# Kernel optimization log

Hardware: AMD Instinct MI355X
Metric: run time of the kernel (lower is better)

Reference implementation:

```python
import jax, jax.numpy as jnp
import numpy as np

EMBED_DIM = 1024
BATCH = 4
SEQ = 2048


def setup_inputs() -> dict:
    key = jax.random.key(0)
    ks = jax.random.split(key, 9)
    E = EMBED_DIM
    s = 1.0 / np.sqrt(E)
    inp = {
        "x": jax.random.normal(ks[0], (BATCH, SEQ, E), dtype=jnp.float32),
        "Wq": jax.random.uniform(ks[1], (E, E), jnp.float32, -s, s),
        "bq": jax.random.uniform(ks[2], (E,), jnp.float32, -s, s),
        "Wk": jax.random.uniform(ks[3], (E, E), jnp.float32, -s, s),
        "bk": jax.random.uniform(ks[4], (E,), jnp.float32, -s, s),
        "Wv": jax.random.uniform(ks[5], (E, E), jnp.float32, -s, s),
        "bv": jax.random.uniform(ks[6], (E,), jnp.float32, -s, s),
        "Wo": jax.random.uniform(ks[7], (E, E), jnp.float32, -s, s),
        "bo": jax.random.uniform(ks[8], (E,), jnp.float32, -s, s),
    }
    return inp


def reference(x, Wq, bq, Wk, bk, Wv, bv, Wo, bo):
    # x: [B, S, E]. Single-head attention over full embed_dim.
    scale = x.shape[-1] ** -0.5
    q = jnp.einsum("bse,ef->bsf", x, Wq.T) + bq
    k = jnp.einsum("bse,ef->bsf", x, Wk.T) + bk
    v = jnp.einsum("bse,ef->bsf", x, Wv.T) + bv
    scores = jnp.einsum("bqe,bke->bqk", q, k) * scale  # [B, S, S]
    attn = jax.nn.softmax(scores, axis=-1)             # dropout p=0 -> identity
    out = jnp.einsum("bqk,bke->bqe", attn, v)
    return jnp.einsum("bse,ef->bsf", out, Wo.T) + bo
```

## Files before the change

### kernel.cpp

```cpp
#include <hip/hip_runtime.h>
#include <hip/hip_bf16.h>


typedef __bf16 bf16_t;
typedef __bf16 bf16x8 __attribute__((ext_vector_type(8)));
typedef __bf16 bf16x4 __attribute__((ext_vector_type(4)));
typedef float  f32x16 __attribute__((ext_vector_type(16)));

__device__ __forceinline__ void async_copy16(const void* g, void* l) {
  __builtin_amdgcn_global_load_lds(
      (const __attribute__((address_space(1))) void*)g,
      (__attribute__((address_space(3))) void*)l, 16, 0, 0);
}

__device__ __forceinline__ void store_out(float* p, float v)  { *p = v; }
__device__ __forceinline__ void store_out(bf16_t* p, float v) { *p = (bf16_t)v; }

#define BM 128
#define BN 128
#define BKT 64

template <typename OutT, int BIAS, int EPI>
__global__ __launch_bounds__(256) void gemm_bt(
    const bf16_t* __restrict__ A, const bf16_t* __restrict__ B,
    OutT* __restrict__ C,
    const float* __restrict__ b0, const float* __restrict__ b1,
    float* __restrict__ rsum, int rsStride,
    int M, int N, int K, int lda, int ldb, int ldc, float scale,
    long long strideA, long long strideB, long long strideC) {
  const int z = blockIdx.z;
  A += (long long)z * strideA;
  B += (long long)z * strideB;
  C += (long long)z * strideC;
  if (EPI >= 1) rsum += (long long)z * rsStride;

  int bx = blockIdx.x, by = blockIdx.y;
  {
    const int GX  = gridDim.x;
    const int id  = by * GX + bx;
    const int per = GX * 8;
    const int grp = id / per;
    const int rem = id - grp * per;
    by = grp * 8 + (rem & 7);
    bx = rem >> 3;
  }

  __shared__ __align__(16) bf16_t As[BM * BKT];
  __shared__ __align__(16) bf16_t Bs[BN * BKT];

  const int t    = threadIdx.x;
  const int lane = t & 63;
  const int w    = t >> 6;
  const int wm   = w & 1;
  const int wn   = w >> 1;
  const int tileM = by * BM;
  const int tileN = bx * BN;

  f32x16 acc[2][2] = {};

  for (int k0 = 0; k0 < K; k0 += BKT) {
#pragma unroll
    for (int i = 0; i < 4; ++i) {
      const int c   = t + 256 * i;
      const int row = c >> 3;
      const int cc  = c & 7;
      const int gcc = cc ^ (row & 7);
      const int ldsbase = ((t & ~63) + 256 * i) * 8;
      async_copy16(A + (long long)(tileM + row) * lda + k0 + gcc * 8, &As[ldsbase]);
      async_copy16(B + (long long)(tileN + row) * ldb + k0 + gcc * 8, &Bs[ldsbase]);
    }
    __syncthreads();

#pragma unroll
    for (int s = 0; s < 4; ++s) {
      const int kc = s + 4 * (lane >> 5);
      bf16x8 af[2], bfr[2];
#pragma unroll
      for (int ti = 0; ti < 2; ++ti) {
        const int row = wm * 64 + ti * 32 + (lane & 31);
        af[ti] = *(const bf16x8*)&As[row * BKT + ((kc ^ (row & 7)) * 8)];
      }
#pragma unroll
      for (int tj = 0; tj < 2; ++tj) {
        const int row = wn * 64 + tj * 32 + (lane & 31);
        bfr[tj] = *(const bf16x8*)&Bs[row * BKT + ((kc ^ (row & 7)) * 8)];
      }
#pragma unroll
      for (int ti = 0; ti < 2; ++ti)
#pragma unroll
        for (int tj = 0; tj < 2; ++tj)
          acc[ti][tj] = __builtin_amdgcn_mfma_f32_32x32x16_bf16(
              af[ti], bfr[tj], acc[ti][tj], 0, 0, 0);
    }
    __syncthreads();
  }

  if (EPI == 0 && BIAS != 3) {
#pragma unroll
    for (int tj = 0; tj < 2; ++tj) {
      const int col = tileN + wn * 64 + tj * 32 + (lane & 31);
      float bv = 0.f;
      if (BIAS == 1) bv = b0[col];
      if (BIAS == 2) bv = (col < 1024 ? b0[col] : b1[col - 1024]);
#pragma unroll
      for (int ti = 0; ti < 2; ++ti) {
        const int rowb = tileM + wm * 64 + ti * 32 + 4 * (lane >> 5);
#pragma unroll
        for (int r = 0; r < 16; ++r) {
          const int row = rowb + (r & 3) + 8 * (r >> 2);
          store_out(&C[(long long)row * ldc + col], acc[ti][tj][r] * scale + bv);
        }
      }
    }
  } else {
    const int col0 = tileN + wn * 64 + (lane & 31);
#pragma unroll
    for (int ti = 0; ti < 2; ++ti) {
      const int rowb = tileM + wm * 64 + ti * 32 + 4 * (lane >> 5);
#pragma unroll
      for (int r = 0; r < 16; ++r) {
        const int row = rowb + (r & 3) + 8 * (r >> 2);
        if (EPI == 1) {
          const float e0 = __expf(acc[ti][0][r] * scale);
          const float e1 = __expf(acc[ti][1][r] * scale);
          store_out(&C[(long long)row * ldc + col0],      e0);
          store_out(&C[(long long)row * ldc + col0 + 32], e1);
          float s = e0 + e1;
          s += __shfl_xor(s, 1);  s += __shfl_xor(s, 2);
          s += __shfl_xor(s, 4);  s += __shfl_xor(s, 8);
          s += __shfl_xor(s, 16);
          if ((lane & 31) == 0) atomicAdd(&rsum[row], s);
        } else if (EPI == 2) {
          const float inv = 1.0f / rsum[row];
          store_out(&C[(long long)row * ldc + col0],      acc[ti][0][r] * inv);
          store_out(&C[(long long)row * ldc + col0 + 32], acc[ti][1][r] * inv);
        } else {
          const float bv = b0[row];
          store_out(&C[(long long)row * ldc + col0],      acc[ti][0][r] * scale + bv);
          store_out(&C[(long long)row * ldc + col0 + 32], acc[ti][1][r] * scale + bv);
        }
      }
    }
  }
}

__global__ __launch_bounds__(256) void cast_all(
    const float4* __restrict__ w0, const float4* __restrict__ w1,
    const float4* __restrict__ w2, const float4* __restrict__ w3,
    const float4* __restrict__ x,
    bf16x4* __restrict__ wdst, bf16x4* __restrict__ xdst,
    float4* __restrict__ rsumv4) {
  const int N4W  = 1 << 18;
  const int BASE = 4 * N4W + (1 << 21);
  const int id = blockIdx.x * 256 + threadIdx.x;
  if (id >= BASE) {
    const int i = id - BASE;
    if (i < 2048) rsumv4[i] = make_float4(0.f, 0.f, 0.f, 0.f);
    return;
  }
  const float4* src;
  bf16x4* dst;
  if (id < 4 * N4W) {
    const int zz = id >> 18;
    src = (zz == 0 ? w0 : zz == 1 ? w1 : zz == 2 ? w2 : w3) + (id & (N4W - 1));
    dst = wdst + id;
  } else {
    const int i = id - 4 * N4W;
    src = x + i;
    dst = xdst + i;
  }
  const float4 v = *src;
  bf16x4 o;
  o[0] = (bf16_t)v.x; o[1] = (bf16_t)v.y; o[2] = (bf16_t)v.z; o[3] = (bf16_t)v.w;
  *dst = o;
}

extern "C" void kernel_launch(void* const* d_in, const int* in_sizes, int n_in,
                              void* d_out, int out_size, void* d_ws, size_t ws_size,
                              hipStream_t stream) {
  const int E = 1024, S = 2048, B = 4;
  const int BS = B * S;

  const float* x  = (const float*)d_in[0];
  const float* Wq = (const float*)d_in[1];
  const float* bq = (const float*)d_in[2];
  const float* Wk = (const float*)d_in[3];
  const float* bk = (const float*)d_in[4];
  const float* Wv = (const float*)d_in[5];
  const float* bv = (const float*)d_in[6];
  const float* Wo = (const float*)d_in[7];
  const float* bo = (const float*)d_in[8];
  float* out = (float*)d_out;

  char* w = (char*)d_ws;
  const size_t MB = 1ull << 20;
  bf16_t* Wqkvb = (bf16_t*)(w + 0 * MB);
  bf16_t* Wvb   = Wqkvb + 2 * E * E;
  bf16_t* Wob   = Wqkvb + 3 * E * E;
  bf16_t* xb    = (bf16_t*)(w + 8 * MB);
  bf16_t* Ob    = (bf16_t*)(w + 8 * MB);
  bf16_t* QKb   = (bf16_t*)(w + 24 * MB);
  bf16_t* VTb   = (bf16_t*)(w + 56 * MB);
  bf16_t* Sb    = (bf16_t*)(w + 72 * MB);
  float*  rsum  = (float*)(w + 104 * MB);

  {
    const int blocks = ((4 << 18) + (1 << 21) + 2048) / 256;
    cast_all<<<blocks, 256, 0, stream>>>(
        (const float4*)Wq, (const float4*)Wk, (const float4*)Wv,
        (const float4*)Wo, (const float4*)x,
        (bf16x4*)Wqkvb, (bf16x4*)xb, (float4*)rsum);
  }

  gemm_bt<bf16_t, 2, 0><<<dim3(2 * E / BN, BS / BM, 1), 256, 0, stream>>>(
      xb, Wqkvb, QKb, bq, bk, nullptr, 0,
      BS, 2 * E, E, E, E, 2 * E, 1.f, 0, 0, 0);

  gemm_bt<bf16_t, 3, 0><<<dim3(BS / BN, E / BM, 1), 256, 0, stream>>>(
      Wvb, xb, VTb, bv, nullptr, nullptr, 0,
      E, BS, E, E, E, BS, 1.f, 0, 0, 0);

  gemm_bt<bf16_t, 0, 1><<<dim3(S / BN, S / BM, B), 256, 0, stream>>>(
      QKb, QKb + E, Sb, nullptr, nullptr, rsum, S,
      S, S, E, 2 * E, 2 * E, S, 0.03125f,
      (long long)S * 2 * E, (long long)S * 2 * E, (long long)S * S);

  gemm_bt<bf16_t, 0, 2><<<dim3(E / BN, S / BM, B), 256, 0, stream>>>(
      Sb, VTb, Ob, nullptr, nullptr, rsum, S,
      S, E, S, S, BS, E, 1.f,
      (long long)S * S, (long long)S, (long long)S * E);

  gemm_bt<float, 1, 0><<<dim3(E / BN, BS / BM, 1), 256, 0, stream>>>(
      Ob, Wob, out, bo, nullptr, nullptr, 0,
      BS, E, E, E, E, E, 1.f, 0, 0, 0);
}
```

Before: 318.5 us.

## Compute softmax row sums via ones-matrix MFMA and defer normalization to output GEMM

The scores epilogue no longer does shuffle reductions and atomicAdd row sums. Instead, the PV kernel gets an extra block column that multiplies the exp-score matrix by an all-ones LDS tile to produce the row sums. Normalization by 1/rowsum moves out of the PV epilogue into the output-projection epilogue, using the identity diag(1/r)·(PV)·Wo. The Q/K and V projections are also merged into one launch, and rsum zeroing is dropped. The trade-offs are extra MFMA work on the ones tile and unnormalized bf16 intermediates.

Result: no change. 321.1 us (+0.8%).

```diff
diff --git a/kernel.cpp b/kernel.cpp
--- a/kernel.cpp
+++ b/kernel.cpp
@@ -20,41 +20,33 @@
 #define BN 128
 #define BKT 64
 
-template <typename OutT, int BIAS, int EPI>
-__global__ __launch_bounds__(256) void gemm_bt(
+__device__ __forceinline__ void supertile(int id, int GX, int& bx, int& by) {
+  const int per = GX * 8;
+  const int grp = id / per;
+  const int rem = id - grp * per;
+  by = grp * 8 + (rem & 7);
+  bx = rem >> 3;
+}
+
+template <typename OutT, int BIAS, int EPI, bool ONES>
+__device__ __forceinline__ void gemm_core(
     const bf16_t* __restrict__ A, const bf16_t* __restrict__ B,
-    OutT* __restrict__ C,
-    const float* __restrict__ b0, const float* __restrict__ b1,
-    float* __restrict__ rsum, int rsStride,
-    int M, int N, int K, int lda, int ldb, int ldc, float scale,
-    long long strideA, long long strideB, long long strideC) {
-  const int z = blockIdx.z;
-  A += (long long)z * strideA;
-  B += (long long)z * strideB;
-  C += (long long)z * strideC;
-  if (EPI >= 1) rsum += (long long)z * rsStride;
-
-  int bx = blockIdx.x, by = blockIdx.y;
-  {
-    const int GX  = gridDim.x;
-    const int id  = by * GX + bx;
-    const int per = GX * 8;
-    const int grp = id / per;
-    const int rem = id - grp * per;
-    by = grp * 8 + (rem & 7);
-    bx = rem >> 3;
-  }
-
-  __shared__ __align__(16) bf16_t As[BM * BKT];
-  __shared__ __align__(16) bf16_t Bs[BN * BKT];
-
+    OutT* __restrict__ C, const float* __restrict__ b0,
+    const float* __restrict__ b1, float* __restrict__ rsum,
+    int K, int lda, int ldb, int ldc, float scale,
+    int tileM, int tileN, bf16_t* As, bf16_t* Bs) {
   const int t    = threadIdx.x;
   const int lane = t & 63;
   const int w    = t >> 6;
   const int wm   = w & 1;
   const int wn   = w >> 1;
-  const int tileM = by * BM;
-  const int tileN = bx * BN;
+
+  if (ONES) {
+    bf16x8 ones8;
+#pragma unroll
+    for (int j = 0; j < 8; ++j) ones8[j] = (bf16_t)1.0f;
+    for (int i = t; i < BN * BKT / 8; i += 256) ((bf16x8*)Bs)[i] = ones8;
+  }
 
   f32x16 acc[2][2] = {};
 
@@ -67,7 +59,8 @@
       const int gcc = cc ^ (row & 7);
       const int ldsbase = ((t & ~63) + 256 * i) * 8;
       async_copy16(A + (long long)(tileM + row) * lda + k0 + gcc * 8, &As[ldsbase]);
-      async_copy16(B + (long long)(tileN + row) * ldb + k0 + gcc * 8, &Bs[ldsbase]);
+      if (!ONES)
+        async_copy16(B + (long long)(tileN + row) * ldb + k0 + gcc * 8, &Bs[ldsbase]);
     }
     __syncthreads();
 
@@ -95,7 +88,56 @@
     __syncthreads();
   }
 
-  if (EPI == 0 && BIAS != 3) {
+  if (EPI == 4) {
+    if (wn == 0 && (lane & 31) == 0) {
+#pragma unroll
+      for (int ti = 0; ti < 2; ++ti) {
+        const int rowb = tileM + wm * 64 + ti * 32 + 4 * (lane >> 5);
+#pragma unroll
+        for (int r = 0; r < 16; ++r)
+          rsum[rowb + (r & 3) + 8 * (r >> 2)] = acc[ti][0][r];
+      }
+    }
+  } else if (EPI == 1) {
+    const int col0 = tileN + wn * 64 + (lane & 31);
+#pragma unroll
+    for (int ti = 0; ti < 2; ++ti) {
+      const int rowb = tileM + wm * 64 + ti * 32 + 4 * (lane >> 5);
+#pragma unroll
+      for (int r = 0; r < 16; ++r) {
+        const int row = rowb + (r & 3) + 8 * (r >> 2);
+        store_out(&C[(long long)row * ldc + col0],      __expf(acc[ti][0][r] * scale));
+        store_out(&C[(long long)row * ldc + col0 + 32], __expf(acc[ti][1][r] * scale));
+      }
+    }
+  } else if (EPI == 3) {
+    const int col0 = tileN + wn * 64 + (lane & 31);
+    const float bv0 = b0[col0], bv1 = b0[col0 + 32];
+#pragma unroll
+    for (int ti = 0; ti < 2; ++ti) {
+      const int rowb = tileM + wm * 64 + ti * 32 + 4 * (lane >> 5);
+#pragma unroll
+      for (int r = 0; r < 16; ++r) {
+        const int row = rowb + (r & 3) + 8 * (r >> 2);
+        const float inv = 1.0f / rsum[row];
+        store_out(&C[(long long)row * ldc + col0],      acc[ti][0][r] * inv + bv0);
+        store_out(&C[(long long)row * ldc + col0 + 32], acc[ti][1][r] * inv + bv1);
+      }
+    }
+  } else if (BIAS == 3) {
+    const int col0 = tileN + wn * 64 + (lane & 31);
+#pragma unroll
+    for (int ti = 0; ti < 2; ++ti) {
+      const int rowb = tileM + wm * 64 + ti * 32 + 4 * (lane >> 5);
+#pragma unroll
+      for (int r = 0; r < 16; ++r) {
+        const int row = rowb + (r & 3) + 8 * (r >> 2);
+        const float bv = b0[row];
+        store_out(&C[(long long)row * ldc + col0],      acc[ti][0][r] * scale + bv);
+        store_out(&C[(long long)row * ldc + col0 + 32], acc[ti][1][r] * scale + bv);
+      }
+    }
+  } else {
 #pragma unroll
     for (int tj = 0; tj < 2; ++tj) {
       const int col = tileN + wn * 64 + tj * 32 + (lane & 31);
@@ -112,52 +154,80 @@
         }
       }
     }
-  } else {
-    const int col0 = tileN + wn * 64 + (lane & 31);
-#pragma unroll
-    for (int ti = 0; ti < 2; ++ti) {
-      const int rowb = tileM + wm * 64 + ti * 32 + 4 * (lane >> 5);
-#pragma unroll
-      for (int r = 0; r < 16; ++r) {
-        const int row = rowb + (r & 3) + 8 * (r >> 2);
-        if (EPI == 1) {
-          const float e0 = __expf(acc[ti][0][r] * scale);
-          const float e1 = __expf(acc[ti][1][r] * scale);
-          store_out(&C[(long long)row * ldc + col0],      e0);
-          store_out(&C[(long long)row * ldc + col0 + 32], e1);
-          float s = e0 + e1;
-          s += __shfl_xor(s, 1);  s += __shfl_xor(s, 2);
-          s += __shfl_xor(s, 4);  s += __shfl_xor(s, 8);
-          s += __shfl_xor(s, 16);
-          if ((lane & 31) == 0) atomicAdd(&rsum[row], s);
-        } else if (EPI == 2) {
-          const float inv = 1.0f / rsum[row];
-          store_out(&C[(long long)row * ldc + col0],      acc[ti][0][r] * inv);
-          store_out(&C[(long long)row * ldc + col0 + 32], acc[ti][1][r] * inv);
-        } else {
-          const float bv = b0[row];
-          store_out(&C[(long long)row * ldc + col0],      acc[ti][0][r] * scale + bv);
-          store_out(&C[(long long)row * ldc + col0 + 32], acc[ti][1][r] * scale + bv);
-        }
-      }
-    }
-  }
+  }
+}
+
+#define LDS_DECL \
+  __shared__ __align__(16) bf16_t As[BM * BKT]; \
+  __shared__ __align__(16) bf16_t Bs[BN * BKT];
+
+__global__ __launch_bounds__(256) void proj_kernel(
+    const bf16_t* __restrict__ xb, const bf16_t* __restrict__ Wqkb,
+    const bf16_t* __restrict__ Wvb, bf16_t* __restrict__ QKb,
+    bf16_t* __restrict__ VTb, const float* __restrict__ bq,
+    const float* __restrict__ bk, const float* __restrict__ bv) {
+  LDS_DECL;
+  const int id = blockIdx.x;
+  if (id < 1024) {
+    int bx, by; supertile(id, 16, bx, by);
+    gemm_core<bf16_t, 2, 0, false>(xb, Wqkb, QKb, bq, bk, nullptr,
+        1024, 1024, 1024, 2048, 1.f, by * 128, bx * 128, As, Bs);
+  } else {
+    int bx, by; supertile(id - 1024, 64, bx, by);
+    gemm_core<bf16_t, 3, 0, false>(Wvb, xb, VTb, bv, nullptr, nullptr,
+        1024, 1024, 1024, 8192, 1.f, by * 128, bx * 128, As, Bs);
+  }
+}
+
+__global__ __launch_bounds__(256) void scores_kernel(
+    const bf16_t* __restrict__ QKb, bf16_t* __restrict__ Sb) {
+  LDS_DECL;
+  const int z = blockIdx.z;
+  const bf16_t* A = QKb + (long long)z * 2048 * 2048;
+  const bf16_t* Bm = A + 1024;
+  bf16_t* C = Sb + (long long)z * 2048 * 2048;
+  int bx, by; supertile(blockIdx.y * 16 + blockIdx.x, 16, bx, by);
+  gemm_core<bf16_t, 0, 1, false>(A, Bm, C, nullptr, nullptr, nullptr,
+      1024, 2048, 2048, 2048, 0.03125f, by * 128, bx * 128, As, Bs);
+}
+
+__global__ __launch_bounds__(256) void pv_kernel(
+    const bf16_t* __restrict__ Sb, const bf16_t* __restrict__ VTb,
+    bf16_t* __restrict__ Ob, float* __restrict__ rsum) {
+  LDS_DECL;
+  const int z = blockIdx.z;
+  const bf16_t* A = Sb + (long long)z * 2048 * 2048;
+  const bf16_t* Bm = VTb + (long long)z * 2048;
+  bf16_t* C = Ob + (long long)z * 2048 * 1024;
+  float* rs = rsum + z * 2048;
+  if (blockIdx.x == 8) {
+    gemm_core<bf16_t, 0, 4, true>(A, nullptr, C, nullptr, nullptr, rs,
+        2048, 2048, 0, 1024, 1.f, blockIdx.y * 128, 0, As, Bs);
+  } else {
+    int bx, by; supertile(blockIdx.y * 8 + blockIdx.x, 8, bx, by);
+    gemm_core<bf16_t, 0, 0, false>(A, Bm, C, nullptr, nullptr, nullptr,
+        2048, 2048, 8192, 1024, 1.f, by * 128, bx * 128, As, Bs);
+  }
+}
+
+__global__ __launch_bounds__(256) void out_kernel(
+    const bf16_t* __restrict__ Ob, const bf16_t* __restrict__ Wob,
+    float* __restrict__ out, const float* __restrict__ bo,
+    const float* __restrict__ rsum) {
+  LDS_DECL;
+  int bx, by; supertile(blockIdx.y * 8 + blockIdx.x, 8, bx, by);
+  gemm_core<float, 1, 3, false>(Ob, Wob, out, bo, nullptr,
+      const_cast<float*>(rsum),
+      1024, 1024, 1024, 1024, 1.f, by * 128, bx * 128, As, Bs);
 }
 
 __global__ __launch_bounds__(256) void cast_all(
     const float4* __restrict__ w0, const float4* __restrict__ w1,
     const float4* __restrict__ w2, const float4* __restrict__ w3,
     const float4* __restrict__ x,
-    bf16x4* __restrict__ wdst, bf16x4* __restrict__ xdst,
-    float4* __restrict__ rsumv4) {
-  const int N4W  = 1 << 18;
-  const int BASE = 4 * N4W + (1 << 21);
+    bf16x4* __restrict__ wdst, bf16x4* __restrict__ xdst) {
+  const int N4W = 1 << 18;
   const int id = blockIdx.x * 256 + threadIdx.x;
-  if (id >= BASE) {
-    const int i = id - BASE;
-    if (i < 2048) rsumv4[i] = make_float4(0.f, 0.f, 0.f, 0.f);
-    return;
-  }
   const float4* src;
   bf16x4* dst;
   if (id < 4 * N4W) {
@@ -194,43 +264,25 @@
 
   char* w = (char*)d_ws;
   const size_t MB = 1ull << 20;
-  bf16_t* Wqkvb = (bf16_t*)(w + 0 * MB);
-  bf16_t* Wvb   = Wqkvb + 2 * E * E;
-  bf16_t* Wob   = Wqkvb + 3 * E * E;
-  bf16_t* xb    = (bf16_t*)(w + 8 * MB);
-  bf16_t* Ob    = (bf16_t*)(w + 8 * MB);
-  bf16_t* QKb   = (bf16_t*)(w + 24 * MB);
-  bf16_t* VTb   = (bf16_t*)(w + 56 * MB);
-  bf16_t* Sb    = (bf16_t*)(w + 72 * MB);
-  float*  rsum  = (float*)(w + 104 * MB);
-
-  {
-    const int blocks = ((4 << 18) + (1 << 21) + 2048) / 256;
-    cast_all<<<blocks, 256, 0, stream>>>(
-        (const float4*)Wq, (const float4*)Wk, (const float4*)Wv,
-        (const float4*)Wo, (const float4*)x,
-        (bf16x4*)Wqkvb, (bf16x4*)xb, (float4*)rsum);
-  }
-
-  gemm_bt<bf16_t, 2, 0><<<dim3(2 * E / BN, BS / BM, 1), 256, 0, stream>>>(
-      xb, Wqkvb, QKb, bq, bk, nullptr, 0,
-      BS, 2 * E, E, E, E, 2 * E, 1.f, 0, 0, 0);
-
-  gemm_bt<bf16_t, 3, 0><<<dim3(BS / BN, E / BM, 1), 256, 0, stream>>>(
-      Wvb, xb, VTb, bv, nullptr, nullptr, 0,
-      E, BS, E, E, E, BS, 1.f, 0, 0, 0);
-
-  gemm_bt<bf16_t, 0, 1><<<dim3(S / BN, S / BM, B), 256, 0, stream>>>(
-      QKb, QKb + E, Sb, nullptr, nullptr, rsum, S,
-      S, S, E, 2 * E, 2 * E, S, 0.03125f,
-      (long long)S * 2 * E, (long long)S * 2 * E, (long long)S * S);
-
-  gemm_bt<bf16_t, 0, 2><<<dim3(E / BN, S / BM, B), 256, 0, stream>>>(
-      Sb, VTb, Ob, nullptr, nullptr, rsum, S,
-      S, E, S, S, BS, E, 1.f,
-      (long long)S * S, (long long)S, (long long)S * E);
-
-  gemm_bt<float, 1, 0><<<dim3(E / BN, BS / BM, 1), 256, 0, stream>>>(
-      Ob, Wob, out, bo, nullptr, nullptr, 0,
-      BS, E, E, E, E, E, 1.f, 0, 0, 0);
-}
+  bf16_t* Wqkb = (bf16_t*)(w + 0 * MB);
+  bf16_t* Wvb  = Wqkb + 2 * E * E;
+  bf16_t* Wob  = Wqkb + 3 * E * E;
+  bf16_t* xb   = (bf16_t*)(w + 8 * MB);
+  bf16_t* Ob   = (bf16_t*)(w + 8 * MB);
+  bf16_t* QKb  = (bf16_t*)(w + 24 * MB);
+  bf16_t* VTb  = (bf16_t*)(w + 56 * MB);
+  bf16_t* Sb   = (bf16_t*)(w + 72 * MB);
+  float*  rsum = (float*)(w + 104 * MB);
+
+  cast_all<<<((4 << 18) + (1 << 21)) / 256, 256, 0, stream>>>(
+      (const float4*)Wq, (const float4*)Wk, (const float4*)Wv,
+      (const float4*)Wo, (const float4*)x, (bf16x4*)Wqkb, (bf16x4*)xb);
+
+  proj_kernel<<<1536, 256, 0, stream>>>(xb, Wqkb, Wvb, QKb, VTb, bq, bk, bv);
+
+  scores_kernel<<<dim3(16, 16, B), 256, 0, stream>>>(QKb, Sb);
+
+  pv_kernel<<<dim3(9, 16, B), 256, 0, stream>>>(Sb, VTb, Ob, rsum);
+
+  out_kernel<<<dim3(8, BS / BM, 1), 256, 0, stream>>>(Ob, Wob, out, bo, rsum);
+}
```
